# Optimization experiments

Measured on AMD Instinct MI355X. Metric: run time of the kernel, lower is better.

Reference implementation:

```python
import jax, jax.numpy as jnp
import numpy as np

D_MODEL = 1024
NUM_HEADS = 16
D_K = D_MODEL // NUM_HEADS


def setup_inputs() -> dict:
    key = jax.random.key(0)
    ks = jax.random.split(key, 7)
    B, S = 4, 2048
    lim = float(np.sqrt(6.0 / (D_MODEL + D_MODEL)))  # xavier uniform
    x = jax.random.normal(ks[0], (B, S, D_MODEL), dtype=jnp.float32)
    w_q = jax.random.uniform(ks[1], (D_MODEL, D_MODEL), jnp.float32, -lim, lim)
    w_k = jax.random.uniform(ks[2], (D_MODEL, D_MODEL), jnp.float32, -lim, lim)
    w_v = jax.random.uniform(ks[3], (D_MODEL, D_MODEL), jnp.float32, -lim, lim)
    w_o = jax.random.uniform(ks[4], (D_MODEL, D_MODEL), jnp.float32, -lim, lim)
    b_o = jnp.zeros((D_MODEL,), jnp.float32)
    ln_g = jnp.ones((D_MODEL,), jnp.float32)
    ln_b = jnp.zeros((D_MODEL,), jnp.float32)
    return {"x": x, "w_q": w_q, "w_k": w_k, "w_v": w_v, "w_o": w_o,
            "b_o": b_o, "ln_g": ln_g, "ln_b": ln_b}


def _layer_norm(y, g, b, eps=1e-5):
    mu = jnp.mean(y, axis=-1, keepdims=True)
    var = jnp.var(y, axis=-1, keepdims=True)
    return (y - mu) * jax.lax.rsqrt(var + eps) * g + b


def reference(x, w_q, w_k, w_v, w_o, b_o, ln_g, ln_b):
    B, S, D = x.shape
    # Linear weights stored torch-style [out, in]: y = x @ W^T
    def proj(w):
        return jnp.einsum('bsd,ed->bse', x, w).reshape(B, S, NUM_HEADS, D_K).transpose(0, 2, 1, 3)
    Q, K, V = proj(w_q), proj(w_k), proj(w_v)  # [B, H, S, d_k]
    scores = jnp.einsum('bhqd,bhkd->bhqk', Q, K) / jnp.sqrt(jnp.float32(D_K))
    attn = jax.nn.softmax(scores, axis=-1)  # dropout identity at eval
    out = jnp.einsum('bhqk,bhkd->bhqd', attn, V)  # [B, H, S, d_k]
    out = out.transpose(0, 2, 1, 3).reshape(B, S, D)
    out = jnp.einsum('bsd,ed->bse', out, w_o) + b_o
    return _layer_norm(x + out, ln_g, ln_b)
```

## Files before the change

### kernel.cpp

```cpp
#include <hip/hip_runtime.h>

typedef __bf16 bf16;
typedef bf16 v8bf __attribute__((ext_vector_type(8)));
typedef bf16 v4bf __attribute__((ext_vector_type(4)));
typedef float v4f __attribute__((ext_vector_type(4)));

#define GAS __attribute__((address_space(1)))
#define LAS __attribute__((address_space(3)))

constexpr int D    = 1024;
constexpr int ROWS = 8192;
constexpr int TILE = 128;

__global__ __launch_bounds__(256) void cast_all(
    const float* __restrict__ x,
    const float* __restrict__ wq, const float* __restrict__ wk,
    const float* __restrict__ wv, const float* __restrict__ wo,
    bf16* __restrict__ xb, bf16* __restrict__ wqb, bf16* __restrict__ wkb,
    bf16* __restrict__ wvb, bf16* __restrict__ wob)
{
    int i = blockIdx.x * 256 + threadIdx.x;
    const float* src; bf16* dst; int off;
    if (i < 2 * 1024 * 1024) { src = x; dst = xb; off = i; }
    else {
        int j = i - 2 * 1024 * 1024;
        int w = j >> 18;
        off = j & ((1 << 18) - 1);
        src = (w == 0) ? wq : (w == 1) ? wk : (w == 2) ? wv : wo;
        dst = (w == 0) ? wqb : (w == 1) ? wkb : (w == 2) ? wvb : wob;
    }
    float4 v = ((const float4*)src)[off];
    v4bf o;
    o[0] = (bf16)v.x; o[1] = (bf16)v.y; o[2] = (bf16)v.z; o[3] = (bf16)v.w;
    ((v4bf*)dst)[off] = o;
}

template<int MODE>
__global__ __launch_bounds__(256) void gemm_bt(
    const bf16* __restrict__ A,
    const bf16* __restrict__ W0, const bf16* __restrict__ W1, const bf16* __restrict__ W2,
    bf16* __restrict__ O0, bf16* __restrict__ O1, bf16* __restrict__ O2,
    float* __restrict__ Of, const float* __restrict__ bias,
    const float* __restrict__ X)
{
    __shared__ bf16 As[2][TILE * 32];
    __shared__ bf16 Bs[2][TILE * 32];

    const int tid  = threadIdx.x;
    const int lane = tid & 63;
    const int wave = tid >> 6;
    const int quad = lane >> 4;
    const int l16  = lane & 15;
    const int wm   = (wave >> 1) * 64;
    const int wn   = (wave & 1) * 64;

    const int z = blockIdx.z;
    const bf16* Bw = (MODE == 0) ? ((z == 0) ? W0 : ((z == 1) ? W1 : W2)) : W0;
    bf16*       Ob = (MODE == 0) ? ((z == 0) ? O0 : ((z == 1) ? O1 : O2)) : O0;

    const long rowA0 = (long)blockIdx.y * TILE;
    const long rowB0 = (long)blockIdx.x * TILE;

    const int stRow = wave * 16 + (lane >> 2);
    const int stCol = (lane & 3) * 8;
    const bf16* gA = A  + (rowA0 + stRow) * D + stCol;
    const bf16* gB = Bw + (rowB0 + stRow) * D + stCol;
    const int ldsOff = wave * 16 * 32;

    const v4f vzero = {0.f, 0.f, 0.f, 0.f};
    v4f acc[4][4];
    #pragma unroll
    for (int i = 0; i < 4; i++)
        #pragma unroll
        for (int j = 0; j < 4; j++) acc[i][j] = vzero;

    for (int k0 = 0; k0 < D; k0 += 64) {
        __syncthreads();
        #pragma unroll
        for (int p = 0; p < 2; ++p)
            #pragma unroll
            for (int i = 0; i < 2; ++i) {
                __builtin_amdgcn_global_load_lds(
                    (const GAS void*)(gA + (long)i * 64 * D + p * 32),
                    (LAS void*)(&As[p][ldsOff + i * 64 * 32]), 16, 0, 0);
                __builtin_amdgcn_global_load_lds(
                    (const GAS void*)(gB + (long)i * 64 * D + p * 32),
                    (LAS void*)(&Bs[p][ldsOff + i * 64 * 32]), 16, 0, 0);
            }
        gA += 64; gB += 64;
        __syncthreads();

        #pragma unroll
        for (int p = 0; p < 2; ++p) {
            v8bf a[4], b[4];
            #pragma unroll
            for (int mi = 0; mi < 4; mi++)
                a[mi] = *(const v8bf*)(&As[p][(wm + mi * 16 + l16) * 32 + quad * 8]);
            #pragma unroll
            for (int ni = 0; ni < 4; ni++)
                b[ni] = *(const v8bf*)(&Bs[p][(wn + ni * 16 + l16) * 32 + quad * 8]);
            #pragma unroll
            for (int mi = 0; mi < 4; mi++)
                #pragma unroll
                for (int ni = 0; ni < 4; ni++)
                    acc[mi][ni] = __builtin_amdgcn_mfma_f32_16x16x32_bf16(a[mi], b[ni], acc[mi][ni], 0, 0, 0);
        }
    }

    const float qscale = 0.125f * 1.44269504f;

    if (MODE == 0 && z == 2) {
        #pragma unroll
        for (int mi = 0; mi < 4; mi++) {
            #pragma unroll
            for (int ni = 0; ni < 4; ni++) {
                const long col = rowB0 + wn + ni * 16 + l16;
                const long h_ = col >> 6, dd = col & 63;
                const long row0 = rowA0 + wm + mi * 16 + quad * 4;
                const long b_ = row0 >> 11, s0 = row0 & 2047;
                v4bf pk;
                #pragma unroll
                for (int r = 0; r < 4; r++) pk[r] = (bf16)acc[mi][ni][r];
                *(v4bf*)(Ob + ((b_ * 16 + h_) * 64 + dd) * 2048 + s0) = pk;
            }
        }
    } else {
        #pragma unroll
        for (int mi = 0; mi < 4; mi++) {
            #pragma unroll
            for (int ni = 0; ni < 4; ni++) {
                const long col = rowB0 + wn + ni * 16 + l16;
                float bv = (MODE == 1) ? bias[col] : 0.f;
                #pragma unroll
                for (int r = 0; r < 4; r++) {
                    const long row = rowA0 + wm + mi * 16 + quad * 4 + r;
                    float v = acc[mi][ni][r];
                    if (MODE == 1) Of[row * D + col] = v + bv + X[row * D + col];
                    else {
                        if (z == 0) v *= qscale;
                        Ob[row * D + col] = (bf16)v;
                    }
                }
            }
        }
    }
}

__global__ __launch_bounds__(256) void attn_kernel(
    const bf16* __restrict__ Q, const bf16* __restrict__ Kg,
    const bf16* __restrict__ VtG, bf16* __restrict__ O)
{
    const int qt = blockIdx.x, h = blockIdx.y, b = blockIdx.z;
    const int tid  = threadIdx.x;
    const int lane = tid & 63;
    const int wave = tid >> 6;
    const int quad = lane >> 4;
    const int l16  = lane & 15;

    __shared__ bf16 Kt[64 * 72];
    __shared__ bf16 Vt[64 * 72];
    __shared__ bf16 Ps[4][32 * 72];

    v8bf qB[2][2];
    #pragma unroll
    for (int qf = 0; qf < 2; qf++) {
        const long qrow = (long)(b * 2048 + qt * 128 + wave * 32 + qf * 16 + l16);
        #pragma unroll
        for (int hh = 0; hh < 2; hh++)
            qB[qf][hh] = *(const v8bf*)(Q + qrow * D + h * 64 + hh * 32 + quad * 8);
    }

    float l_acc[2] = {0.f, 0.f};
    v4f o_acc[2][4];
    const v4f vzero = {0.f, 0.f, 0.f, 0.f};
    #pragma unroll
    for (int qf = 0; qf < 2; qf++)
        #pragma unroll
        for (int nf = 0; nf < 4; nf++) o_acc[qf][nf] = vzero;

    const int sC = (tid & 7) * 8;
    const int iR = tid >> 3;

    const bf16* kLane = Kg  + (long)b * 2048 * D + h * 64 + sC + (long)iR * D;
    const bf16* vLane = VtG + (long)(b * 16 + h) * 64 * 2048 + sC + (long)iR * 2048;
    bf16* ktW = Kt + iR * 72 + sC;
    bf16* vtW = Vt + iR * 72 + sC;

    v8bf kpre[2], vpre[2];
    kpre[0] = *(const v8bf*)(kLane);
    kpre[1] = *(const v8bf*)(kLane + 32 * D);
    vpre[0] = *(const v8bf*)(vLane);
    vpre[1] = *(const v8bf*)(vLane + 32 * 2048);
    kLane += 64 * D;
    vLane += 64;

    for (int kt = 0; kt < 32; ++kt) {
        __syncthreads();
        *(v8bf*)(ktW)            = kpre[0];
        *(v8bf*)(ktW + 32 * 72)  = kpre[1];
        *(v8bf*)(vtW)            = vpre[0];
        *(v8bf*)(vtW + 32 * 72)  = vpre[1];
        __syncthreads();

        if (kt + 1 < 32) {
            kpre[0] = *(const v8bf*)(kLane);
            kpre[1] = *(const v8bf*)(kLane + 32 * D);
            vpre[0] = *(const v8bf*)(vLane);
            vpre[1] = *(const v8bf*)(vLane + 32 * 2048);
            kLane += 64 * D;
            vLane += 64;
        }

        v4f st[4][2];
        #pragma unroll
        for (int kf = 0; kf < 4; kf++) {
            v8bf kA0 = *(const v8bf*)(Kt + (kf * 16 + l16) * 72 + quad * 8);
            v8bf kA1 = *(const v8bf*)(Kt + (kf * 16 + l16) * 72 + 32 + quad * 8);
            #pragma unroll
            for (int qf = 0; qf < 2; qf++) {
                v4f t = vzero;
                t = __builtin_amdgcn_mfma_f32_16x16x32_bf16(kA0, qB[qf][0], t, 0, 0, 0);
                t = __builtin_amdgcn_mfma_f32_16x16x32_bf16(kA1, qB[qf][1], t, 0, 0, 0);
                st[kf][qf] = t;
            }
        }

        #pragma unroll
        for (int qf = 0; qf < 2; qf++)
            #pragma unroll
            for (int kf = 0; kf < 4; kf++) {
                v4bf pk;
                #pragma unroll
                for (int r = 0; r < 4; r++) {
                    float p = __builtin_amdgcn_exp2f(st[kf][qf][r]);
                    l_acc[qf] += p;
                    pk[r] = (bf16)p;
                }
                *(v4bf*)(&Ps[wave][(qf * 16 + l16) * 72 + kf * 16 + quad * 4]) = pk;
            }

        #pragma unroll
        for (int ks = 0; ks < 2; ++ks) {
            v8bf vb[4];
            #pragma unroll
            for (int nf = 0; nf < 4; nf++)
                vb[nf] = *(const v8bf*)(Vt + (nf * 16 + l16) * 72 + ks * 32 + quad * 8);
            #pragma unroll
            for (int qf = 0; qf < 2; qf++) {
                v8bf pa = *(const v8bf*)(&Ps[wave][(qf * 16 + l16) * 72 + ks * 32 + quad * 8]);
                #pragma unroll
                for (int nf = 0; nf < 4; nf++)
                    o_acc[qf][nf] = __builtin_amdgcn_mfma_f32_16x16x32_bf16(pa, vb[nf], o_acc[qf][nf], 0, 0, 0);
            }
        }
    }

    #pragma unroll
    for (int qf = 0; qf < 2; qf++) {
        float l = l_acc[qf];
        l += __shfl_xor(l, 16);
        l += __shfl_xor(l, 32);
        l_acc[qf] = l;
    }

    #pragma unroll
    for (int qf = 0; qf < 2; qf++) {
        float inv[4];
        #pragma unroll
        for (int r = 0; r < 4; r++) {
            const int src = (quad << 4) | (quad * 4 + r);
            inv[r] = 1.f / __shfl(l_acc[qf], src);
        }
        const long orow = (long)(b * 2048 + qt * 128 + wave * 32 + qf * 16 + quad * 4);
        #pragma unroll
        for (int nf = 0; nf < 4; nf++)
            #pragma unroll
            for (int r = 0; r < 4; r++)
                O[(orow + r) * D + h * 64 + nf * 16 + l16] = (bf16)(o_acc[qf][nf][r] * inv[r]);
    }
}

__global__ __launch_bounds__(256) void ln_kernel(
    const float* __restrict__ g, const float* __restrict__ beta,
    float* __restrict__ out)
{
    const int row = blockIdx.x;
    const int t = threadIdx.x;
    const int lane = t & 63, wave = t >> 6;
    const long base = (long)row * D + t * 4;

    float4 yv = *(const float4*)(out + base);
    float y0 = yv.x, y1 = yv.y, y2 = yv.z, y3 = yv.w;
    float s1 = y0 + y1 + y2 + y3;
    float s2 = y0*y0 + y1*y1 + y2*y2 + y3*y3;
    #pragma unroll
    for (int off = 1; off < 64; off <<= 1) {
        s1 += __shfl_xor(s1, off);
        s2 += __shfl_xor(s2, off);
    }
    __shared__ float r1[4], r2[4];
    if (lane == 0) { r1[wave] = s1; r2[wave] = s2; }
    __syncthreads();
    float S1 = r1[0] + r1[1] + r1[2] + r1[3];
    float S2 = r2[0] + r2[1] + r2[2] + r2[3];
    float mu  = S1 * (1.f / 1024.f);
    float var = S2 * (1.f / 1024.f) - mu * mu;
    float rsd = rsqrtf(var + 1e-5f);

    float4 gv = *(const float4*)(g + t * 4);
    float4 bv = *(const float4*)(beta + t * 4);
    float4 o;
    o.x = (y0 - mu) * rsd * gv.x + bv.x;
    o.y = (y1 - mu) * rsd * gv.y + bv.y;
    o.z = (y2 - mu) * rsd * gv.z + bv.z;
    o.w = (y3 - mu) * rsd * gv.w + bv.w;
    *(float4*)(out + base) = o;
}

extern "C" void kernel_launch(void* const* d_in, const int* in_sizes, int n_in,
                              void* d_out, int out_size, void* d_ws, size_t ws_size,
                              hipStream_t stream)
{
    const float* x   = (const float*)d_in[0];
    const float* wq  = (const float*)d_in[1];
    const float* wk  = (const float*)d_in[2];
    const float* wv  = (const float*)d_in[3];
    const float* wo  = (const float*)d_in[4];
    const float* bo  = (const float*)d_in[5];
    const float* lng = (const float*)d_in[6];
    const float* lnb = (const float*)d_in[7];
    float* out = (float*)d_out;

    char* ws = (char*)d_ws;
    bf16* xb  = (bf16*)(ws);
    bf16* wqb = (bf16*)(ws + (size_t)16 * 1024 * 1024);
    bf16* wkb = wqb + 1024 * 1024;
    bf16* wvb = wkb + 1024 * 1024;
    bf16* wob = wvb + 1024 * 1024;
    bf16* Qb  = (bf16*)(ws + (size_t)24 * 1024 * 1024);
    bf16* Kb  = Qb + (size_t)ROWS * D;
    bf16* VtG = Kb + (size_t)ROWS * D;
    bf16* Ab  = VtG + (size_t)ROWS * D;

    cast_all<<<12288, 256, 0, stream>>>(x, wq, wk, wv, wo,
                                        xb, wqb, wkb, wvb, wob);

    dim3 gqkv(D / TILE, ROWS / TILE, 3);
    gemm_bt<0><<<gqkv, 256, 0, stream>>>(xb, wqb, wkb, wvb, Qb, Kb, VtG,
                                         nullptr, nullptr, nullptr);

    attn_kernel<<<dim3(16, 16, 4), 256, 0, stream>>>(Qb, Kb, VtG, Ab);

    dim3 gout(D / TILE, ROWS / TILE, 1);
    gemm_bt<1><<<gout, 256, 0, stream>>>(Ab, wob, nullptr, nullptr,
                                         nullptr, nullptr, nullptr, out, bo, x);

    ln_kernel<<<8192, 256, 0, stream>>>(lng, lnb, out);
}
```

Measured before the change: 316.5 us.

## Keep attention probabilities in registers via shuffles instead of LDS staging

```diff
diff --git a/kernel.cpp b/kernel.cpp
--- a/kernel.cpp
+++ b/kernel.cpp
@@ -159,7 +159,6 @@
 
     __shared__ bf16 Kt[64 * 72];
     __shared__ bf16 Vt[64 * 72];
-    __shared__ bf16 Ps[4][32 * 72];
 
     v8bf qB[2][2];
     #pragma unroll
@@ -171,12 +170,12 @@
     }
 
     float l_acc[2] = {0.f, 0.f};
-    v4f o_acc[2][4];
+    v4f o_t[4][2];
     const v4f vzero = {0.f, 0.f, 0.f, 0.f};
     #pragma unroll
-    for (int qf = 0; qf < 2; qf++)
-        #pragma unroll
-        for (int nf = 0; nf < 4; nf++) o_acc[qf][nf] = vzero;
+    for (int mf = 0; mf < 4; mf++)
+        #pragma unroll
+        for (int qf = 0; qf < 2; qf++) o_t[mf][qf] = vzero;
 
     const int sC = (tid & 7) * 8;
     const int iR = tid >> 3;
@@ -194,6 +193,10 @@
     kLane += 64 * D;
     vLane += 64;
 
+    const int s0 = ((quad & 1) << 5) + l16;
+    const int s1 = s0 + 16;
+    const bool hiKf = (quad >> 1) & 1;
+
     for (int kt = 0; kt < 32; ++kt) {
         __syncthreads();
         *(v8bf*)(ktW)            = kpre[0];
@@ -202,11 +205,14 @@
         *(v8bf*)(vtW + 32 * 72)  = vpre[1];
         __syncthreads();
 
-        if (kt + 1 < 32) {
-            kpre[0] = *(const v8bf*)(kLane);
-            kpre[1] = *(const v8bf*)(kLane + 32 * D);
-            vpre[0] = *(const v8bf*)(vLane);
-            vpre[1] = *(const v8bf*)(vLane + 32 * 2048);
+        {
+            const int ktn = (kt + 1) & 31;
+            const bf16* kp = kLane + (long)(ktn - kt - 1) * 64 * D;
+            const bf16* vp = vLane + (ktn - kt - 1) * 64;
+            kpre[0] = *(const v8bf*)(kp);
+            kpre[1] = *(const v8bf*)(kp + 32 * D);
+            vpre[0] = *(const v8bf*)(vp);
+            vpre[1] = *(const v8bf*)(vp + 32 * 2048);
             kLane += 64 * D;
             vLane += 64;
         }
@@ -225,10 +231,11 @@
             }
         }
 
-        #pragma unroll
-        for (int qf = 0; qf < 2; qf++)
-            #pragma unroll
-            for (int kf = 0; kf < 4; kf++) {
+        int2 pk2[4][2];
+        #pragma unroll
+        for (int kf = 0; kf < 4; kf++)
+            #pragma unroll
+            for (int qf = 0; qf < 2; qf++) {
                 v4bf pk;
                 #pragma unroll
                 for (int r = 0; r < 4; r++) {
@@ -236,47 +243,52 @@
                     l_acc[qf] += p;
                     pk[r] = (bf16)p;
                 }
-                *(v4bf*)(&Ps[wave][(qf * 16 + l16) * 72 + kf * 16 + quad * 4]) = pk;
+                pk2[kf][qf] = *(int2*)&pk;
             }
 
         #pragma unroll
         for (int ks = 0; ks < 2; ++ks) {
-            v8bf vb[4];
-            #pragma unroll
-            for (int nf = 0; nf < 4; nf++)
-                vb[nf] = *(const v8bf*)(Vt + (nf * 16 + l16) * 72 + ks * 32 + quad * 8);
+            v8bf va[4];
+            #pragma unroll
+            for (int mf = 0; mf < 4; mf++)
+                va[mf] = *(const v8bf*)(Vt + (mf * 16 + l16) * 72 + ks * 32 + quad * 8);
             #pragma unroll
             for (int qf = 0; qf < 2; qf++) {
-                v8bf pa = *(const v8bf*)(&Ps[wave][(qf * 16 + l16) * 72 + ks * 32 + quad * 8]);
-                #pragma unroll
-                for (int nf = 0; nf < 4; nf++)
-                    o_acc[qf][nf] = __builtin_amdgcn_mfma_f32_16x16x32_bf16(pa, vb[nf], o_acc[qf][nf], 0, 0, 0);
-            }
-        }
-    }
-
+                int a0 = __shfl(pk2[2*ks][qf].x, s0),   a1 = __shfl(pk2[2*ks][qf].y, s0);
+                int a2 = __shfl(pk2[2*ks][qf].x, s1),   a3 = __shfl(pk2[2*ks][qf].y, s1);
+                int b0 = __shfl(pk2[2*ks+1][qf].x, s0), b1 = __shfl(pk2[2*ks+1][qf].y, s0);
+                int b2 = __shfl(pk2[2*ks+1][qf].x, s1), b3 = __shfl(pk2[2*ks+1][qf].y, s1);
+                int4 w;
+                w.x = hiKf ? b0 : a0; w.y = hiKf ? b1 : a1;
+                w.z = hiKf ? b2 : a2; w.w = hiKf ? b3 : a3;
+                v8bf pb = *(v8bf*)&w;
+                #pragma unroll
+                for (int mf = 0; mf < 4; mf++)
+                    o_t[mf][qf] = __builtin_amdgcn_mfma_f32_16x16x32_bf16(va[mf], pb, o_t[mf][qf], 0, 0, 0);
+            }
+        }
+    }
+
+    float inv[2];
     #pragma unroll
     for (int qf = 0; qf < 2; qf++) {
         float l = l_acc[qf];
         l += __shfl_xor(l, 16);
         l += __shfl_xor(l, 32);
-        l_acc[qf] = l;
-    }
-
+        inv[qf] = 1.f / l;
+    }
+
+    const long qrow0 = (long)(b * 2048 + qt * 128 + wave * 32);
     #pragma unroll
     for (int qf = 0; qf < 2; qf++) {
-        float inv[4];
-        #pragma unroll
-        for (int r = 0; r < 4; r++) {
-            const int src = (quad << 4) | (quad * 4 + r);
-            inv[r] = 1.f / __shfl(l_acc[qf], src);
-        }
-        const long orow = (long)(b * 2048 + qt * 128 + wave * 32 + qf * 16 + quad * 4);
-        #pragma unroll
-        for (int nf = 0; nf < 4; nf++)
-            #pragma unroll
-            for (int r = 0; r < 4; r++)
-                O[(orow + r) * D + h * 64 + nf * 16 + l16] = (bf16)(o_acc[qf][nf][r] * inv[r]);
+        const long rbase = (qrow0 + qf * 16 + l16) * D + h * 64;
+        #pragma unroll
+        for (int mf = 0; mf < 4; mf++) {
+            v4bf ov;
+            #pragma unroll
+            for (int r = 0; r < 4; r++) ov[r] = (bf16)(o_t[mf][qf][r] * inv[qf]);
+            *(v4bf*)(O + rbase + mf * 16 + quad * 4) = ov;
+        }
     }
 }
 
```

Result: slower. 333.7 us (+5.4%).
